# Kernel optimization log

Hardware: AMD Instinct MI355X
Metric: run time of the kernel (lower is better)

The kernel has to match this reference:

```python
import jax, jax.numpy as jnp
import numpy as np

VOCAB = 5000
B, T = 32, 1024

def setup_inputs() -> dict:
    key = jax.random.key(0)
    k1, k2 = jax.random.split(key)
    x = jax.random.randint(k1, (B, T), 0, VOCAB)  # token ids
    # nn.Linear weight: [out_features, in_features] = [V, V]
    W = jax.random.normal(k2, (VOCAB, VOCAB), dtype=jnp.float32) * (1.0 / np.sqrt(VOCAB))
    return {"x": x, "W": W}

def reference(x, W):
    # torch: out = one_hot(x, V).float() @ W.T
    # one-hot row e_i @ W.T selects column i of W.T == W[:, i],
    # i.e. out[b, t, :] = W[:, x[b, t]] -- a pure row-gather of W.T.
    return jnp.take(W.T, x, axis=0)  # [B, T, V]
```

## Files before the change

kernel.cpp:

```cpp
#include <hip/hip_runtime.h>

#define VOCAB 5000
#define TTOK  16
#define JCH   2048
#define NTT   313

typedef float f32x4 __attribute__((ext_vector_type(4)));

__global__ void zero_kernel(int* __restrict__ ptr, int n) {
    int i = blockIdx.x * blockDim.x + threadIdx.x;
    if (i < n) ptr[i] = 0;
}

__global__ void hist_kernel(const int* __restrict__ x, int* __restrict__ counts, int n) {
    int i = blockIdx.x * blockDim.x + threadIdx.x;
    if (i < n) atomicAdd(&counts[x[i]], 1);
}

__global__ void scan_kernel(const int* __restrict__ counts, int* __restrict__ offs) {
    __shared__ int part[1024];
    const int tid = threadIdx.x;
    const int base = tid * 5;
    int local[5];
    int sum = 0;
#pragma unroll
    for (int k = 0; k < 5; ++k) {
        int idx = base + k;
        int v = (idx < VOCAB) ? counts[idx] : 0;
        local[k] = sum;
        sum += v;
    }
    part[tid] = sum;
    __syncthreads();
    for (int off = 1; off < 1024; off <<= 1) {
        int v = 0;
        if (tid >= off) v = part[tid - off];
        __syncthreads();
        if (tid >= off) part[tid] += v;
        __syncthreads();
    }
    const int prev = (tid > 0) ? part[tid - 1] : 0;
#pragma unroll
    for (int k = 0; k < 5; ++k) {
        int idx = base + k;
        if (idx < VOCAB) offs[idx] = prev + local[k];
    }
    if (tid == 1023) offs[VOCAB] = part[1023];
}

__global__ void scatter_kernel(const int* __restrict__ x, const int* __restrict__ offs,
                               int* __restrict__ cursor, int* __restrict__ sorted_pk, int n) {
    int i = blockIdx.x * blockDim.x + threadIdx.x;
    if (i < n) {
        int t = x[i];
        int d = atomicAdd(&cursor[t], 1);
        sorted_pk[offs[t] + d] = (i << 13) | t;
    }
}

__global__ __launch_bounds__(1024) void fused_gather_kernel(
        const float* __restrict__ W,
        const int* __restrict__ offs,
        const int* __restrict__ sorted_pk,
        float* __restrict__ out) {
    __shared__ float tileT[TTOK][JCH];
    const int j0 = blockIdx.x * JCH;
    const int t0 = blockIdx.y * TTOK;
    const int jcnt = min(JCH, VOCAB - j0);
    const int tcnt = min(TTOK, VOCAB - t0);
    const int tid = threadIdx.x;

    const int begin = offs[t0];
    const int end   = offs[t0 + tcnt];
    if (begin == end) return;

    const int nc4   = tcnt >> 2;
    const int csh   = (tcnt == TTOK) ? 2 : 1;
    const int cmask = nc4 - 1;
    const int total = jcnt * nc4;
    for (int idx = tid; idx < total; idx += 1024) {
        const int jr = idx >> csh;
        const int c  = idx & cmask;
        f32x4 v = *reinterpret_cast<const f32x4*>(
            W + (size_t)(j0 + jr) * VOCAB + t0 + c * 4);
        tileT[c * 4 + 0][jr] = v.x;
        tileT[c * 4 + 1][jr] = v.y;
        tileT[c * 4 + 2][jr] = v.z;
        tileT[c * 4 + 3][jr] = v.w;
    }
    __syncthreads();

    const int wid  = tid >> 6;
    const int lane = tid & 63;
    const int f0 = lane * 4;
    const int nfull    = jcnt >> 8;
    const int remlanes = (jcnt & 255) >> 2;

    int i = begin + wid;
    if (i >= end) return;
    int pk = sorted_pk[i];
    for (;;) {
        const int inext = i + 16;
        int pk_next = 0;
        if (inext < end) pk_next = sorted_pk[inext];

        const int p  = pk >> 13;
        const int tt = (pk & 8191) - t0;
        const float* __restrict__ srow = &tileT[tt][0];
        float* __restrict__ drow = out + (size_t)p * VOCAB + j0;
#pragma unroll
        for (int s = 0; s < 8; ++s) {
            if (s < nfull) {
                f32x4 v = *reinterpret_cast<const f32x4*>(srow + f0 + s * 256);
                __builtin_nontemporal_store(
                    v, reinterpret_cast<f32x4*>(drow + f0 + s * 256));
            }
        }
        if (lane < remlanes) {
            f32x4 v = *reinterpret_cast<const f32x4*>(srow + f0 + nfull * 256);
            __builtin_nontemporal_store(
                v, reinterpret_cast<f32x4*>(drow + f0 + nfull * 256));
        }
        if (inext >= end) break;
        i = inext;
        pk = pk_next;
    }
}

__global__ void gather_cols_kernel(const float* __restrict__ W,
                                   const int* __restrict__ idx,
                                   float* __restrict__ out) {
    const int p = blockIdx.x;
    const int token = idx[p];
    for (int v = threadIdx.x; v < VOCAB; v += blockDim.x)
        out[(size_t)p * VOCAB + v] = W[(size_t)v * VOCAB + token];
}

extern "C" void kernel_launch(void* const* d_in, const int* in_sizes, int n_in,
                              void* d_out, int out_size, void* d_ws, size_t ws_size,
                              hipStream_t stream) {
    const int*   x = (const int*)d_in[0];
    const float* W = (const float*)d_in[1];
    float* out = (float*)d_out;
    const int npos = in_sizes[0];

    int* counts = (int*)d_ws;
    int* cursor = counts + VOCAB;
    int* offs   = cursor + VOCAB;
    int* sorted = offs + VOCAB + 1;
    const size_t need = (size_t)(3 * VOCAB + 1 + npos) * sizeof(int);

    if (ws_size >= need) {
        zero_kernel<<<(2 * VOCAB + 255) / 256, 256, 0, stream>>>(counts, 2 * VOCAB);
        hist_kernel<<<(npos + 255) / 256, 256, 0, stream>>>(x, counts, npos);
        scan_kernel<<<1, 1024, 0, stream>>>(counts, offs);
        scatter_kernel<<<(npos + 255) / 256, 256, 0, stream>>>(x, offs, cursor, sorted, npos);
        dim3 grid((VOCAB + JCH - 1) / JCH, (VOCAB + TTOK - 1) / TTOK);
        fused_gather_kernel<<<grid, 1024, 0, stream>>>(W, offs, sorted, out);
    } else {
        gather_cols_kernel<<<npos, 256, 0, stream>>>(W, x, out);
    }
}
```

Measured before the change: 186.7 us.

## Fuse counting sort into one single-block kernel and shrink gather column chunk

The four preprocessing launches (zero, histogram, scan, scatter) become one single-workgroup kernel that keeps counts and cursors in shared memory, which removes launch overhead and global atomics. The gather kernel's column chunk drops from 2048 to 1024, with the LDS row stride padded to 1028 to cut bank conflicts and to allow more blocks per CU. The cost is that one workgroup now processes all 32K tokens serially for the histogram and scatter, and the gather grid gains more blocks that each reload their W tile.

```diff
diff --git a/kernel.cpp b/kernel.cpp
--- a/kernel.cpp
+++ b/kernel.cpp
@@ -2,31 +2,31 @@
 
 #define VOCAB 5000
 #define TTOK  16
-#define JCH   2048
-#define NTT   313
+#define JCH   1024
+#define LSTR  1028
 
 typedef float f32x4 __attribute__((ext_vector_type(4)));
 
-__global__ void zero_kernel(int* __restrict__ ptr, int n) {
-    int i = blockIdx.x * blockDim.x + threadIdx.x;
-    if (i < n) ptr[i] = 0;
-}
-
-__global__ void hist_kernel(const int* __restrict__ x, int* __restrict__ counts, int n) {
-    int i = blockIdx.x * blockDim.x + threadIdx.x;
-    if (i < n) atomicAdd(&counts[x[i]], 1);
-}
-
-__global__ void scan_kernel(const int* __restrict__ counts, int* __restrict__ offs) {
+__global__ __launch_bounds__(1024) void sort_kernel(
+        const int* __restrict__ x, int n,
+        int* __restrict__ offs_g, int* __restrict__ sorted_pk) {
+    __shared__ int cnt[VOCAB];
     __shared__ int part[1024];
     const int tid = threadIdx.x;
+
+    for (int i = tid; i < VOCAB; i += 1024) cnt[i] = 0;
+    __syncthreads();
+
+    for (int i = tid; i < n; i += 1024) atomicAdd(&cnt[x[i]], 1);
+    __syncthreads();
+
     const int base = tid * 5;
     int local[5];
     int sum = 0;
 #pragma unroll
     for (int k = 0; k < 5; ++k) {
         int idx = base + k;
-        int v = (idx < VOCAB) ? counts[idx] : 0;
+        int v = (idx < VOCAB) ? cnt[idx] : 0;
         local[k] = sum;
         sum += v;
     }
@@ -43,18 +43,19 @@
 #pragma unroll
     for (int k = 0; k < 5; ++k) {
         int idx = base + k;
-        if (idx < VOCAB) offs[idx] = prev + local[k];
+        if (idx < VOCAB) {
+            int o = prev + local[k];
+            offs_g[idx] = o;
+            cnt[idx] = o;
+        }
     }
-    if (tid == 1023) offs[VOCAB] = part[1023];
-}
+    if (tid == 1023) offs_g[VOCAB] = part[1023];
+    __syncthreads();
 
-__global__ void scatter_kernel(const int* __restrict__ x, const int* __restrict__ offs,
-                               int* __restrict__ cursor, int* __restrict__ sorted_pk, int n) {
-    int i = blockIdx.x * blockDim.x + threadIdx.x;
-    if (i < n) {
+    for (int i = tid; i < n; i += 1024) {
         int t = x[i];
-        int d = atomicAdd(&cursor[t], 1);
-        sorted_pk[offs[t] + d] = (i << 13) | t;
+        int slot = atomicAdd(&cnt[t], 1);
+        sorted_pk[slot] = (i << 13) | t;
     }
 }
 
@@ -63,7 +64,7 @@
         const int* __restrict__ offs,
         const int* __restrict__ sorted_pk,
         float* __restrict__ out) {
-    __shared__ float tileT[TTOK][JCH];
+    __shared__ float tileT[TTOK][LSTR];
     const int j0 = blockIdx.x * JCH;
     const int t0 = blockIdx.y * TTOK;
     const int jcnt = min(JCH, VOCAB - j0);
@@ -109,7 +110,7 @@
         const float* __restrict__ srow = &tileT[tt][0];
         float* __restrict__ drow = out + (size_t)p * VOCAB + j0;
 #pragma unroll
-        for (int s = 0; s < 8; ++s) {
+        for (int s = 0; s < 4; ++s) {
             if (s < nfull) {
                 f32x4 v = *reinterpret_cast<const f32x4*>(srow + f0 + s * 256);
                 __builtin_nontemporal_store(
@@ -144,17 +145,12 @@
     float* out = (float*)d_out;
     const int npos = in_sizes[0];
 
-    int* counts = (int*)d_ws;
-    int* cursor = counts + VOCAB;
-    int* offs   = cursor + VOCAB;
+    int* offs   = (int*)d_ws;
     int* sorted = offs + VOCAB + 1;
-    const size_t need = (size_t)(3 * VOCAB + 1 + npos) * sizeof(int);
+    const size_t need = (size_t)(VOCAB + 1 + npos) * sizeof(int);
 
     if (ws_size >= need) {
-        zero_kernel<<<(2 * VOCAB + 255) / 256, 256, 0, stream>>>(counts, 2 * VOCAB);
-        hist_kernel<<<(npos + 255) / 256, 256, 0, stream>>>(x, counts, npos);
-        scan_kernel<<<1, 1024, 0, stream>>>(counts, offs);
-        scatter_kernel<<<(npos + 255) / 256, 256, 0, stream>>>(x, offs, cursor, sorted, npos);
+        sort_kernel<<<1, 1024, 0, stream>>>(x, npos, offs, sorted);
         dim3 grid((VOCAB + JCH - 1) / JCH, (VOCAB + TTOK - 1) / TTOK);
         fused_gather_kernel<<<grid, 1024, 0, stream>>>(W, offs, sorted, out);
     } else {
```

After: 206.4 us. 1.11x slower.

## Double-buffer W sub-tiles in LDS and vectorise histogram/scatter kernels

Applied to the files above, without the earlier changes.

The gather kernel splits each 16-token tile into two 8-token sub-tiles with two LDS buffers. Loads of the second sub-tile are issued before stores of the first, so global reads overlap output writes. The histogram and scatter kernels process four token ids per thread with vector loads, and the zeroing kernel is replaced by hipMemsetAsync. The empty-range early exit is gone, so W tiles are loaded even when no tokens map to them.

```diff
diff --git a/kernel.cpp b/kernel.cpp
--- a/kernel.cpp
+++ b/kernel.cpp
@@ -2,19 +2,24 @@
 
 #define VOCAB 5000
 #define TTOK  16
+#define TSUB  8
 #define JCH   2048
-#define NTT   313
 
 typedef float f32x4 __attribute__((ext_vector_type(4)));
-
-__global__ void zero_kernel(int* __restrict__ ptr, int n) {
-    int i = blockIdx.x * blockDim.x + threadIdx.x;
-    if (i < n) ptr[i] = 0;
-}
+typedef int   i32x4 __attribute__((ext_vector_type(4)));
 
 __global__ void hist_kernel(const int* __restrict__ x, int* __restrict__ counts, int n) {
     int i = blockIdx.x * blockDim.x + threadIdx.x;
-    if (i < n) atomicAdd(&counts[x[i]], 1);
+    int base = i * 4;
+    if (base + 3 < n) {
+        i32x4 v = *reinterpret_cast<const i32x4*>(x + base);
+        atomicAdd(&counts[v.x], 1);
+        atomicAdd(&counts[v.y], 1);
+        atomicAdd(&counts[v.z], 1);
+        atomicAdd(&counts[v.w], 1);
+    } else {
+        for (int k = base; k < n; ++k) atomicAdd(&counts[x[k]], 1);
+    }
 }
 
 __global__ void scan_kernel(const int* __restrict__ counts, int* __restrict__ offs) {
@@ -51,10 +56,20 @@
 __global__ void scatter_kernel(const int* __restrict__ x, const int* __restrict__ offs,
                                int* __restrict__ cursor, int* __restrict__ sorted_pk, int n) {
     int i = blockIdx.x * blockDim.x + threadIdx.x;
-    if (i < n) {
-        int t = x[i];
-        int d = atomicAdd(&cursor[t], 1);
-        sorted_pk[offs[t] + d] = (i << 13) | t;
+    int base = i * 4;
+    if (base + 3 < n) {
+        i32x4 v = *reinterpret_cast<const i32x4*>(x + base);
+        int d;
+        d = atomicAdd(&cursor[v.x], 1); sorted_pk[offs[v.x] + d] = ((base + 0) << 13) | v.x;
+        d = atomicAdd(&cursor[v.y], 1); sorted_pk[offs[v.y] + d] = ((base + 1) << 13) | v.y;
+        d = atomicAdd(&cursor[v.z], 1); sorted_pk[offs[v.z] + d] = ((base + 2) << 13) | v.z;
+        d = atomicAdd(&cursor[v.w], 1); sorted_pk[offs[v.w] + d] = ((base + 3) << 13) | v.w;
+    } else {
+        for (int k = base; k < n; ++k) {
+            int t = x[k];
+            int d = atomicAdd(&cursor[t], 1);
+            sorted_pk[offs[t] + d] = (k << 13) | t;
+        }
     }
 }
 
@@ -63,67 +78,90 @@
         const int* __restrict__ offs,
         const int* __restrict__ sorted_pk,
         float* __restrict__ out) {
-    __shared__ float tileT[TTOK][JCH];
+    __shared__ float buf[2][TSUB][JCH];
     const int j0 = blockIdx.x * JCH;
     const int t0 = blockIdx.y * TTOK;
     const int jcnt = min(JCH, VOCAB - j0);
     const int tcnt = min(TTOK, VOCAB - t0);
-    const int tid = threadIdx.x;
-
-    const int begin = offs[t0];
-    const int end   = offs[t0 + tcnt];
-    if (begin == end) return;
-
-    const int nc4   = tcnt >> 2;
-    const int csh   = (tcnt == TTOK) ? 2 : 1;
-    const int cmask = nc4 - 1;
-    const int total = jcnt * nc4;
-    for (int idx = tid; idx < total; idx += 1024) {
-        const int jr = idx >> csh;
-        const int c  = idx & cmask;
-        f32x4 v = *reinterpret_cast<const f32x4*>(
-            W + (size_t)(j0 + jr) * VOCAB + t0 + c * 4);
-        tileT[c * 4 + 0][jr] = v.x;
-        tileT[c * 4 + 1][jr] = v.y;
-        tileT[c * 4 + 2][jr] = v.z;
-        tileT[c * 4 + 3][jr] = v.w;
-    }
-    __syncthreads();
-
+    const int nsub = tcnt >> 3;
+    const int tid  = threadIdx.x;
     const int wid  = tid >> 6;
     const int lane = tid & 63;
-    const int f0 = lane * 4;
+    const int f0   = lane * 4;
     const int nfull    = jcnt >> 8;
     const int remlanes = (jcnt & 255) >> 2;
 
-    int i = begin + wid;
-    if (i >= end) return;
-    int pk = sorted_pk[i];
-    for (;;) {
-        const int inext = i + 16;
-        int pk_next = 0;
-        if (inext < end) pk_next = sorted_pk[inext];
-
-        const int p  = pk >> 13;
-        const int tt = (pk & 8191) - t0;
-        const float* __restrict__ srow = &tileT[tt][0];
-        float* __restrict__ drow = out + (size_t)p * VOCAB + j0;
-#pragma unroll
-        for (int s = 0; s < 8; ++s) {
-            if (s < nfull) {
-                f32x4 v = *reinterpret_cast<const f32x4*>(srow + f0 + s * 256);
+    f32x4 r[4];
+
+    auto issue_loads = [&](int ts) {
+#pragma unroll
+        for (int k = 0; k < 4; ++k) {
+            const int q = tid + k * 1024;
+            const int jr = q >> 1, c = q & 1;
+            if (jr < jcnt)
+                r[k] = *reinterpret_cast<const f32x4*>(
+                    W + (size_t)(j0 + jr) * VOCAB + ts + c * 4);
+        }
+    };
+    auto write_lds = [&](int sb) {
+#pragma unroll
+        for (int k = 0; k < 4; ++k) {
+            const int q = tid + k * 1024;
+            const int jr = q >> 1, c = q & 1;
+            if (jr < jcnt) {
+                buf[sb][c * 4 + 0][jr] = r[k].x;
+                buf[sb][c * 4 + 1][jr] = r[k].y;
+                buf[sb][c * 4 + 2][jr] = r[k].z;
+                buf[sb][c * 4 + 3][jr] = r[k].w;
+            }
+        }
+    };
+    auto store_sub = [&](int sb, int ts) {
+        const int begin = offs[ts];
+        const int end   = offs[ts + TSUB];
+        int i = begin + wid;
+        if (i >= end) return;
+        int pk = sorted_pk[i];
+        for (;;) {
+            const int inext = i + 16;
+            int pk_next = 0;
+            if (inext < end) pk_next = sorted_pk[inext];
+
+            const int p  = pk >> 13;
+            const int tt = (pk & 8191) - ts;
+            const float* __restrict__ srow = &buf[sb][tt][0];
+            float* __restrict__ drow = out + (size_t)p * VOCAB + j0;
+#pragma unroll
+            for (int s = 0; s < 8; ++s) {
+                if (s < nfull) {
+                    f32x4 v = *reinterpret_cast<const f32x4*>(srow + f0 + s * 256);
+                    __builtin_nontemporal_store(
+                        v, reinterpret_cast<f32x4*>(drow + f0 + s * 256));
+                }
+            }
+            if (lane < remlanes) {
+                f32x4 v = *reinterpret_cast<const f32x4*>(srow + f0 + nfull * 256);
                 __builtin_nontemporal_store(
-                    v, reinterpret_cast<f32x4*>(drow + f0 + s * 256));
+                    v, reinterpret_cast<f32x4*>(drow + f0 + nfull * 256));
             }
-        }
-        if (lane < remlanes) {
-            f32x4 v = *reinterpret_cast<const f32x4*>(srow + f0 + nfull * 256);
-            __builtin_nontemporal_store(
-                v, reinterpret_cast<f32x4*>(drow + f0 + nfull * 256));
-        }
-        if (inext >= end) break;
-        i = inext;
-        pk = pk_next;
+            if (inext >= end) break;
+            i = inext;
+            pk = pk_next;
+        }
+    };
+
+    issue_loads(t0);
+    write_lds(0);
+    __syncthreads();
+
+    if (nsub == 2) {
+        issue_loads(t0 + TSUB);
+        store_sub(0, t0);
+        write_lds(1);
+        __syncthreads();
+        store_sub(1, t0 + TSUB);
+    } else {
+        store_sub(0, t0);
     }
 }
 
@@ -151,10 +189,11 @@
     const size_t need = (size_t)(3 * VOCAB + 1 + npos) * sizeof(int);
 
     if (ws_size >= need) {
-        zero_kernel<<<(2 * VOCAB + 255) / 256, 256, 0, stream>>>(counts, 2 * VOCAB);
-        hist_kernel<<<(npos + 255) / 256, 256, 0, stream>>>(x, counts, npos);
+        hipMemsetAsync(counts, 0, (size_t)2 * VOCAB * sizeof(int), stream);
+        const int n4blocks = ((npos + 3) / 4 + 255) / 256;
+        hist_kernel<<<n4blocks, 256, 0, stream>>>(x, counts, npos);
         scan_kernel<<<1, 1024, 0, stream>>>(counts, offs);
-        scatter_kernel<<<(npos + 255) / 256, 256, 0, stream>>>(x, offs, cursor, sorted, npos);
+        scatter_kernel<<<n4blocks, 256, 0, stream>>>(x, offs, cursor, sorted, npos);
         dim3 grid((VOCAB + JCH - 1) / JCH, (VOCAB + TTOK - 1) / TTOK);
         fused_gather_kernel<<<grid, 1024, 0, stream>>>(W, offs, sorted, out);
     } else {
```

Measured after the change: 194.0 us. 1.04x slower.
